# Performance work log

Measured on AMD Instinct MI355X. Metric: run time of the kernel, lower is better.

Reference implementation:

```python
import jax, jax.numpy as jnp
import numpy as np

EPS = 1e-8


def eq_linear(z, weight, bias):
    # EqualisedLinear: runtime weight scale c = 1/sqrt(in_features)
    c = 1.0 / np.sqrt(weight.shape[1]).astype(np.float32)
    return z @ (weight * c).T + bias


def mod_conv(x, w_raw, s, demodulate):
    # w_raw: [out, in, k, k], s: [b, in]
    out_c, in_c, k, _ = w_raw.shape
    c = 1.0 / np.sqrt(in_c * k * k).astype(np.float32)
    wt = w_raw * c
    # per-sample modulated weights: [b, out, in, k, k]
    ws = wt[None] * s[:, None, :, None, None]
    if demodulate:
        sigma_inv = jax.lax.rsqrt(jnp.sum(ws * ws, axis=(2, 3, 4), keepdims=True) + EPS)
        ws = ws * sigma_inv
    def conv1(xi, wi):
        return jax.lax.conv_general_dilated(
            xi[None], wi, window_strides=(1, 1), padding='SAME',
            dimension_numbers=('NCHW', 'OIHW', 'NCHW'))[0]
    return jax.vmap(conv1)(x, ws)


def lrelu(v):
    return jax.nn.leaky_relu(v, 0.2)


def style_block(x, w, noise, style_w, style_b, conv_w, noise_scale, bias):
    s = eq_linear(w, style_w, style_b)
    x = mod_conv(x, conv_w, s, demodulate=True)
    x = x + noise_scale[None, :, None, None] * noise
    return lrelu(x + bias[None, :, None, None])


def to_rgb(x, w, style_w, style_b, conv_w, bias):
    s = eq_linear(w, style_w, style_b)
    x = mod_conv(x, conv_w, s, demodulate=False)
    return lrelu(x + bias[None, :, None, None])


def setup_inputs() -> dict:
    key = jax.random.key(0)
    ks = jax.random.split(key, 16)
    B, C, H, W = 16, 512, 64, 64
    D = 512
    OUT = 3
    return {
        'x': jax.random.normal(ks[0], (B, C, H, W), jnp.float32),
        'w': jax.random.normal(ks[1], (B, D), jnp.float32),
        'noise1': jax.random.normal(ks[2], (B, 1, H, W), jnp.float32),
        'noise2': jax.random.normal(ks[3], (B, 1, H, W), jnp.float32),
        'sb1_style_w': jax.random.normal(ks[4], (C, D), jnp.float32),
        'sb1_style_b': jnp.ones((C,), jnp.float32),
        'sb1_conv_w': jax.random.normal(ks[5], (C, C, 3, 3), jnp.float32),
        'sb1_noise_scale': 0.1 * jax.random.normal(ks[6], (1,), jnp.float32),
        'sb1_bias': 0.1 * jax.random.normal(ks[7], (C,), jnp.float32),
        'sb2_style_w': jax.random.normal(ks[8], (C, D), jnp.float32),
        'sb2_style_b': jnp.ones((C,), jnp.float32),
        'sb2_conv_w': jax.random.normal(ks[9], (C, C, 3, 3), jnp.float32),
        'sb2_noise_scale': 0.1 * jax.random.normal(ks[10], (1,), jnp.float32),
        'sb2_bias': 0.1 * jax.random.normal(ks[11], (C,), jnp.float32),
        'rgb_style_w': jax.random.normal(ks[12], (C, D), jnp.float32),
        'rgb_style_b': jnp.ones((C,), jnp.float32),
        'rgb_conv_w': jax.random.normal(ks[13], (OUT, C, 1, 1), jnp.float32),
        'rgb_bias': 0.1 * jax.random.normal(ks[14], (OUT,), jnp.float32),
    }


def reference(x, w, noise1, noise2,
              sb1_style_w, sb1_style_b, sb1_conv_w, sb1_noise_scale, sb1_bias,
              sb2_style_w, sb2_style_b, sb2_conv_w, sb2_noise_scale, sb2_bias,
              rgb_style_w, rgb_style_b, rgb_conv_w, rgb_bias):
    x = style_block(x, w, noise1, sb1_style_w, sb1_style_b, sb1_conv_w, sb1_noise_scale, sb1_bias)
    x = style_block(x, w, noise2, sb2_style_w, sb2_style_b, sb2_conv_w, sb2_noise_scale, sb2_bias)
    rgb = to_rgb(x, w, rgb_style_w, rgb_style_b, rgb_conv_w, rgb_bias)
    return (x, rgb)
```

## Files before the change

kernel.cpp:

```cpp
#include <hip/hip_runtime.h>
#include <hip/hip_bf16.h>

typedef float f32x4 __attribute__((ext_vector_type(4)));
typedef short short8 __attribute__((ext_vector_type(8)));

#define CC   512
#define PIX  4096
#define XHROWBYTES 4224
#define XHBYTES    16896

__device__ __forceinline__ unsigned short f2bf(float f){
    __hip_bfloat16 h = __float2bfloat16(f);
    return __builtin_bit_cast(unsigned short, h);
}
__device__ __forceinline__ unsigned pk2(float a, float b){
    return (unsigned)f2bf(a) | ((unsigned)f2bf(b) << 16);
}
__device__ __forceinline__ void mfma_bf16(f32x4& c, short8 a, short8 b){
    asm("v_mfma_f32_16x16x32_bf16 %0, %1, %2, %0" : "+v"(c) : "v"(a), "v"(b));
}

__global__ void k_style3(const float* __restrict__ w,
                         const float* __restrict__ sw0, const float* __restrict__ sb0, float* __restrict__ o0,
                         const float* __restrict__ sw1, const float* __restrict__ sb1, float* __restrict__ o1,
                         const float* __restrict__ sw2, const float* __restrict__ sb2, float* __restrict__ o2){
    __shared__ float wl[512];
    const int b = blockIdx.x, l = blockIdx.y, tid = threadIdx.x;
    const float* sw = (l==0) ? sw0 : (l==1 ? sw1 : sw2);
    const float* sb = (l==0) ? sb0 : (l==1 ? sb1 : sb2);
    float* so       = (l==0) ? o0  : (l==1 ? o1  : o2);
    wl[tid]       = w[b*512 + tid];
    wl[tid + 256] = w[b*512 + 256 + tid];
    __syncthreads();
    const float c = 0.044194173824159216f;
    for (int cc = tid; cc < 512; cc += 256){
        const float4* row = (const float4*)(sw + cc*512);
        float acc = 0.f;
        #pragma unroll 4
        for (int dd = 0; dd < 128; ++dd){
            float4 v = row[dd];
            float4 wv = ((const float4*)wl)[dd];
            acc += v.x*wv.x + v.y*wv.y + v.z*wv.z + v.w*wv.w;
        }
        so[b*512 + cc] = acc * c + sb[cc];
    }
}

__global__ void k_w2(const float* __restrict__ cw1, const float* __restrict__ cw2,
                     float* __restrict__ w2_1, float* __restrict__ w2_2){
    int gid = blockIdx.x*256 + threadIdx.x;
    int layer = gid >> 18; int r = gid & 262143;
    const float* cw = layer ? cw2 : cw1;
    float* w2 = layer ? w2_2 : w2_1;
    const float c2 = 1.0f/4608.0f;
    const float* p = cw + r*9;
    float sum = 0.f;
    #pragma unroll
    for (int t=0;t<9;++t){ float v = p[t]; sum += v*v; }
    w2[r] = sum * c2;
}

__global__ void k_demod2(const float* __restrict__ w21, const float* __restrict__ w22,
                         const float* __restrict__ s1,  const float* __restrict__ s2,
                         float* __restrict__ d1, float* __restrict__ d2){
    __shared__ float s2l[512];
    const int b = blockIdx.x, l = blockIdx.y, o = threadIdx.x;
    const float* w2 = l ? w22 : w21;
    const float* s  = l ? s2  : s1;
    float* d        = l ? d2  : d1;
    float sv = s[b*512 + o]; s2l[o] = sv*sv;
    __syncthreads();
    const float4* row = (const float4*)(w2 + o*512);
    const float4* sq  = (const float4*)s2l;
    float acc = 0.f;
    #pragma unroll 4
    for (int i=0;i<128;++i){
        float4 a = row[i], bq = sq[i];
        acc += a.x*bq.x + a.y*bq.y + a.z*bq.z + a.w*bq.w;
    }
    d[b*512 + o] = rsqrtf(acc + 1e-8f);
}

__global__ void k_pack(const float* __restrict__ cw1, const float* __restrict__ cw2,
                       uint4* __restrict__ wpk1, uint4* __restrict__ wpk2){
    int gid = blockIdx.x*256 + threadIdx.x;
    int layer = (gid >= 294912);
    int r = layer ? gid - 294912 : gid;
    const float* cw = layer ? cw2 : cw1;
    uint4* dst = layer ? wpk2 : wpk1;
    int lane = r & 63;
    int ofr  = (r>>6) & 31;
    int cb   = (r>>11) & 15;
    int t    = r>>15;
    int o  = ofr*16 + (lane&15);
    int i0 = cb*32 + (lane>>4)*8;
    const float c = 0.014731391274719738f;
    const float* src = cw + (o*512 + i0)*9 + t;
    float f[8];
    #pragma unroll
    for (int j=0;j<8;++j) f[j] = src[j*9]*c;
    uint4 wv;
    wv.x = pk2(f[0],f[1]); wv.y = pk2(f[2],f[3]);
    wv.z = pk2(f[4],f[5]); wv.w = pk2(f[6],f[7]);
    dst[r] = wv;
}

__global__ __launch_bounds__(256, 2)
void k_conv(const float* __restrict__ x, float* __restrict__ y,
            const unsigned short* __restrict__ wpk, const float* __restrict__ s,
            const float* __restrict__ dmod, const float* __restrict__ noise,
            const float* __restrict__ nsp, const float* __restrict__ bias){
    __shared__ __align__(16) char smem[35840];
    char* xh0 = smem;
    char* xh1 = smem + XHBYTES;
    float* s_lds = (float*)(smem + 2*XHBYTES);

    const int tid  = threadIdx.x;
    const int obp  = blockIdx.x;
    const int rb   = blockIdx.y;
    const int b    = blockIdx.z;
    const int r0   = rb*2;
    const int lane = tid & 63;
    const int wv   = tid >> 6;
    const int ln15 = lane & 15;
    const int hi   = lane >> 4;

    const float* xb = x + (size_t)b * (512*PIX);

    s_lds[tid]       = s[b*512 + tid];
    s_lds[tid + 256] = s[b*512 + 256 + tid];
    __syncthreads();

    f32x4 acc[4][8];
    #pragma unroll
    for (int mi=0;mi<4;++mi)
        #pragma unroll
        for (int ni=0;ni<8;++ni) acc[mi][ni] = (f32x4)(0.f);

    unsigned bcol[3][4];
    #pragma unroll
    for (int dxi=0; dxi<3; ++dxi)
        #pragma unroll
        for (int ni=0; ni<4; ++ni){
            int xcol = ni*16 + ln15 + dxi;
            unsigned a = (unsigned)(xcol*64 + hi*16);
            a ^= (unsigned)(((xcol>>1)&3)<<4);
            bcol[dxi][ni] = a;
        }

    const int scol   = tid & 63;
    const int schunk = (tid>>6) & 3;
    unsigned wcol = (unsigned)((scol+1)*64 + schunk*16);
    wcol ^= (unsigned)((((scol+1)>>1)&3)<<4);

    auto stage = [&](int cb, char* dst){
        float sv[8];
        #pragma unroll
        for (int j=0;j<8;++j) sv[j] = s_lds[cb*32 + schunk*8 + j];
        const float* srcbase = xb + (size_t)(cb*32 + schunk*8)*PIX + scol;
        #pragma unroll
        for (int row=0; row<4; ++row){
            int gr = r0 - 1 + row;
            uint4 wq = make_uint4(0u,0u,0u,0u);
            if (0 <= gr && gr < 64){
                const float* sp = srcbase + gr*64;
                float f0 = sp[0*PIX]*sv[0], f1 = sp[1*PIX]*sv[1];
                float f2 = sp[2*PIX]*sv[2], f3 = sp[3*PIX]*sv[3];
                float f4 = sp[4*PIX]*sv[4], f5 = sp[5*PIX]*sv[5];
                float f6 = sp[6*PIX]*sv[6], f7 = sp[7*PIX]*sv[7];
                wq.x = pk2(f0,f1); wq.y = pk2(f2,f3);
                wq.z = pk2(f4,f5); wq.w = pk2(f6,f7);
            }
            *(uint4*)(dst + row*XHROWBYTES + wcol) = wq;
        }
        if (tid < 32){
            int row = tid>>3; int hc = (tid&4) ? 65 : 0; int ck = tid&3;
            unsigned a = (unsigned)((row*66 + hc)*64 + ck*16);
            a ^= (unsigned)(((hc>>1)&3)<<4);
            *(uint4*)(dst + a) = make_uint4(0u,0u,0u,0u);
        }
    };

    stage(0, xh0);

    const short8* wpf = (const short8*)wpk + (size_t)(obp*16 + wv*4)*64 + lane;

    #pragma unroll 2
    for (int cb=0; cb<16; ++cb){
        __syncthreads();
        if (cb+1 < 16) stage(cb+1, (cb&1) ? xh0 : xh1);
        const char* cur = (cb&1) ? xh1 : xh0;
        const short8* wp = wpf + (size_t)cb*(32*64);
        #pragma unroll
        for (int t=0; t<9; ++t){
            const int dxi = t%3;
            short8 Af[4];
            #pragma unroll
            for (int mi=0;mi<4;++mi) Af[mi] = wp[(size_t)t*(16*32*64) + mi*64];
            const char* rbase0 = cur + (t/3)*XHROWBYTES;
            const char* rbase1 = rbase0 + XHROWBYTES;
            short8 Bf[8];
            #pragma unroll
            for (int ni=0;ni<4;++ni) Bf[ni]   = *(const short8*)(rbase0 + bcol[dxi][ni]);
            #pragma unroll
            for (int ni=0;ni<4;++ni) Bf[4+ni] = *(const short8*)(rbase1 + bcol[dxi][ni]);
            #pragma unroll
            for (int ni=0;ni<8;++ni)
                #pragma unroll
                for (int mi=0;mi<4;++mi)
                    mfma_bf16(acc[mi][ni], Af[mi], Bf[ni]);
        }
    }

    const int obase = obp*256 + wv*64;
    const float nsv = nsp[0];
    const float* dgl = dmod + b*512 + obase;
    const float* bgl = bias + obase;
    float nz[8];
    #pragma unroll
    for (int ni=0;ni<8;++ni){
        int row = r0 + (ni>>2);
        nz[ni] = nsv * noise[b*PIX + row*64 + (ni&3)*16 + ln15];
    }
    float* yb = y + ((size_t)(b*512 + obase))*PIX;
    #pragma unroll
    for (int mi=0;mi<4;++mi){
        float dv[4], bv[4];
        #pragma unroll
        for (int r=0;r<4;++r){
            int ol = mi*16 + hi*4 + r;
            dv[r] = dgl[ol]; bv[r] = bgl[ol];
        }
        #pragma unroll
        for (int ni=0;ni<8;++ni){
            int row = r0 + (ni>>2);
            int col = (ni&3)*16 + ln15;
            #pragma unroll
            for (int r=0;r<4;++r){
                float v = acc[mi][ni][r]*dv[r] + nz[ni] + bv[r];
                v = fmaxf(v, 0.2f*v);
                yb[(size_t)(mi*16 + hi*4 + r)*PIX + row*64 + col] = v;
            }
        }
    }
}

__global__ void k_rgb(const float* __restrict__ x2, const float* __restrict__ srgb,
                      const float* __restrict__ cw, const float* __restrict__ bias,
                      float* __restrict__ out){
    __shared__ float4 wr[512];
    const int b = blockIdx.x, tid = threadIdx.x;
    const float c = 0.044194173824159216f;
    for (int cc = tid; cc < 512; cc += 256){
        float sc = srgb[b*512 + cc]*c;
        wr[cc] = make_float4(cw[cc]*sc, cw[512+cc]*sc, cw[1024+cc]*sc, 0.f);
    }
    __syncthreads();
    int px = blockIdx.y*256 + tid;
    const float* xp = x2 + (size_t)b*(512*PIX) + px;
    float a0=0.f, a1=0.f, a2=0.f;
    #pragma unroll 4
    for (int i=0;i<512;++i){
        float xv = xp[(size_t)i*PIX];
        float4 wv = wr[i];
        a0 += wv.x*xv; a1 += wv.y*xv; a2 += wv.z*xv;
    }
    a0 += bias[0]; a1 += bias[1]; a2 += bias[2];
    out[(size_t)(b*3+0)*PIX + px] = fmaxf(a0, 0.2f*a0);
    out[(size_t)(b*3+1)*PIX + px] = fmaxf(a1, 0.2f*a1);
    out[(size_t)(b*3+2)*PIX + px] = fmaxf(a2, 0.2f*a2);
}

extern "C" void kernel_launch(void* const* d_in, const int* in_sizes, int n_in,
                              void* d_out, int out_size, void* d_ws, size_t ws_size,
                              hipStream_t stream) {
    const float* x    = (const float*)d_in[0];
    const float* w    = (const float*)d_in[1];
    const float* n1   = (const float*)d_in[2];
    const float* n2   = (const float*)d_in[3];
    const float* s1w  = (const float*)d_in[4];
    const float* s1b  = (const float*)d_in[5];
    const float* c1w  = (const float*)d_in[6];
    const float* ns1  = (const float*)d_in[7];
    const float* b1   = (const float*)d_in[8];
    const float* s2w  = (const float*)d_in[9];
    const float* s2b  = (const float*)d_in[10];
    const float* c2w  = (const float*)d_in[11];
    const float* ns2  = (const float*)d_in[12];
    const float* b2   = (const float*)d_in[13];
    const float* rw   = (const float*)d_in[14];
    const float* rbv  = (const float*)d_in[15];
    const float* rcw  = (const float*)d_in[16];
    const float* rbias= (const float*)d_in[17];

    float* out_x   = (float*)d_out;
    float* out_rgb = out_x + (size_t)16*512*PIX;

    char* ws = (char*)d_ws;
    float* s1   = (float*)(ws + 0);
    float* s2   = (float*)(ws + 32768);
    float* srgb = (float*)(ws + 65536);
    float* d1   = (float*)(ws + 98304);
    float* d2   = (float*)(ws + 131072);
    float* w21  = (float*)(ws + 163840);
    float* w22  = (float*)(ws + 163840 + 1048576);
    unsigned short* wp1 = (unsigned short*)(ws + 2260992);
    unsigned short* wp2 = wp1 + 2359296;
    float* x1   = (float*)(ws + 11698176);

    k_style3<<<dim3(16,3), 256, 0, stream>>>(w, s1w, s1b, s1, s2w, s2b, s2, rw, rbv, srgb);
    k_w2<<<2048, 256, 0, stream>>>(c1w, c2w, w21, w22);
    k_pack<<<2304, 256, 0, stream>>>(c1w, c2w, (uint4*)wp1, (uint4*)wp2);
    k_demod2<<<dim3(16,2), 512, 0, stream>>>(w21, w22, s1, s2, d1, d2);

    dim3 cg(2, 32, 16);
    k_conv<<<cg, 256, 0, stream>>>(x,  x1,    wp1, s1, d1, n1, ns1, b1);
    k_conv<<<cg, 256, 0, stream>>>(x1, out_x, wp2, s2, d2, n2, ns2, b2);
    k_rgb<<<dim3(16,16), 256, 0, stream>>>(out_x, srgb, rcw, rbias, out_rgb);
}
```

Measured before the change: 797.0 us.

## Pre-stage modulated bf16 halo tiles globally and DMA them into LDS

Adds a separate k_stage_g pass that applies the style scale, converts x to bf16 and writes swizzled, padded 6-row halo tiles to workspace. k_conv then copies its 4-row window into LDS with global_load_lds direct transfers rather than doing per-thread fp32 loads, scaling and packing. This is meant to remove the staging ALU work and the redundant fp32 reads from the conv's main loop. The cost is an extra kernel launch and global write/read traffic for the packed tiles. It also hoists the first tap's weight loads ahead of the staging call, and the layer-1 output now goes to out_x instead of a separate buffer.

Result: slower. 839.5 us (+5.3%).

```diff
diff --git a/kernel.cpp b/kernel.cpp
--- a/kernel.cpp
+++ b/kernel.cpp
@@ -4,10 +4,11 @@
 typedef float f32x4 __attribute__((ext_vector_type(4)));
 typedef short short8 __attribute__((ext_vector_type(8)));
 
-#define CC   512
-#define PIX  4096
-#define XHROWBYTES 4224
-#define XHBYTES    16896
+#define CC    512
+#define PIX   4096
+#define ROWB  4224
+#define TILE6 25344
+#define TILE4 16896
 
 __device__ __forceinline__ unsigned short f2bf(float f){
     __hip_bfloat16 h = __float2bfloat16(f);
@@ -18,6 +19,11 @@
 }
 __device__ __forceinline__ void mfma_bf16(f32x4& c, short8 a, short8 b){
     asm("v_mfma_f32_16x16x32_bf16 %0, %1, %2, %0" : "+v"(c) : "v"(a), "v"(b));
+}
+__device__ __forceinline__ void gl_lds16(const void* g, void* l){
+    __builtin_amdgcn_global_load_lds(
+        (const __attribute__((address_space(1))) unsigned int*)g,
+        (__attribute__((address_space(3))) unsigned int*)l, 16, 0, 0);
 }
 
 __global__ void k_style3(const float* __restrict__ w,
@@ -105,61 +111,28 @@
     dst[r] = wv;
 }
 
-__global__ __launch_bounds__(256, 2)
-void k_conv(const float* __restrict__ x, float* __restrict__ y,
-            const unsigned short* __restrict__ wpk, const float* __restrict__ s,
-            const float* __restrict__ dmod, const float* __restrict__ noise,
-            const float* __restrict__ nsp, const float* __restrict__ bias){
-    __shared__ __align__(16) char smem[35840];
-    char* xh0 = smem;
-    char* xh1 = smem + XHBYTES;
-    float* s_lds = (float*)(smem + 2*XHBYTES);
-
-    const int tid  = threadIdx.x;
-    const int obp  = blockIdx.x;
-    const int rb   = blockIdx.y;
-    const int b    = blockIdx.z;
-    const int r0   = rb*2;
-    const int lane = tid & 63;
-    const int wv   = tid >> 6;
-    const int ln15 = lane & 15;
-    const int hi   = lane >> 4;
-
-    const float* xb = x + (size_t)b * (512*PIX);
-
+__global__ void k_stage_g(const float* __restrict__ x, const float* __restrict__ s,
+                          char* __restrict__ xpg){
+    __shared__ float s_lds[512];
+    const int tid = threadIdx.x;
+    const int rb = blockIdx.x, b = blockIdx.y;
+    const int r0 = rb*4;
     s_lds[tid]       = s[b*512 + tid];
     s_lds[tid + 256] = s[b*512 + 256 + tid];
     __syncthreads();
-
-    f32x4 acc[4][8];
-    #pragma unroll
-    for (int mi=0;mi<4;++mi)
-        #pragma unroll
-        for (int ni=0;ni<8;++ni) acc[mi][ni] = (f32x4)(0.f);
-
-    unsigned bcol[3][4];
-    #pragma unroll
-    for (int dxi=0; dxi<3; ++dxi)
-        #pragma unroll
-        for (int ni=0; ni<4; ++ni){
-            int xcol = ni*16 + ln15 + dxi;
-            unsigned a = (unsigned)(xcol*64 + hi*16);
-            a ^= (unsigned)(((xcol>>1)&3)<<4);
-            bcol[dxi][ni] = a;
-        }
-
     const int scol   = tid & 63;
     const int schunk = (tid>>6) & 3;
     unsigned wcol = (unsigned)((scol+1)*64 + schunk*16);
     wcol ^= (unsigned)((((scol+1)>>1)&3)<<4);
-
-    auto stage = [&](int cb, char* dst){
+    const float* xb = x + (size_t)b * (512*PIX);
+    for (int cb=0; cb<16; ++cb){
+        char* dst = xpg + ((size_t)((b*16 + rb)*16 + cb))*TILE6;
         float sv[8];
         #pragma unroll
         for (int j=0;j<8;++j) sv[j] = s_lds[cb*32 + schunk*8 + j];
         const float* srcbase = xb + (size_t)(cb*32 + schunk*8)*PIX + scol;
         #pragma unroll
-        for (int row=0; row<4; ++row){
+        for (int row=0; row<6; ++row){
             int gr = r0 - 1 + row;
             uint4 wq = make_uint4(0u,0u,0u,0u);
             if (0 <= gr && gr < 64){
@@ -171,14 +144,62 @@
                 wq.x = pk2(f0,f1); wq.y = pk2(f2,f3);
                 wq.z = pk2(f4,f5); wq.w = pk2(f6,f7);
             }
-            *(uint4*)(dst + row*XHROWBYTES + wcol) = wq;
-        }
-        if (tid < 32){
+            *(uint4*)(dst + row*ROWB + wcol) = wq;
+        }
+        if (tid < 48){
             int row = tid>>3; int hc = (tid&4) ? 65 : 0; int ck = tid&3;
             unsigned a = (unsigned)((row*66 + hc)*64 + ck*16);
             a ^= (unsigned)(((hc>>1)&3)<<4);
             *(uint4*)(dst + a) = make_uint4(0u,0u,0u,0u);
         }
+    }
+}
+
+__global__ __launch_bounds__(256, 2)
+void k_conv(const char* __restrict__ xpg, float* __restrict__ y,
+            const unsigned short* __restrict__ wpk,
+            const float* __restrict__ dmod, const float* __restrict__ noise,
+            const float* __restrict__ nsp, const float* __restrict__ bias){
+    __shared__ __align__(16) char smem[2*TILE4];
+    char* xh0 = smem;
+    char* xh1 = smem + TILE4;
+
+    const int tid  = threadIdx.x;
+    const int obp  = blockIdx.x;
+    const int rb   = blockIdx.y;
+    const int b    = blockIdx.z;
+    const int r0   = rb*2;
+    const int lane = tid & 63;
+    const int wv   = tid >> 6;
+    const int ln15 = lane & 15;
+    const int hi   = lane >> 4;
+
+    f32x4 acc[4][8];
+    #pragma unroll
+    for (int mi=0;mi<4;++mi)
+        #pragma unroll
+        for (int ni=0;ni<8;++ni) acc[mi][ni] = (f32x4)(0.f);
+
+    unsigned bcol[3][4];
+    #pragma unroll
+    for (int dxi=0; dxi<3; ++dxi)
+        #pragma unroll
+        for (int ni=0; ni<4; ++ni){
+            int xcol = ni*16 + ln15 + dxi;
+            unsigned a = (unsigned)(xcol*64 + hi*16);
+            a ^= (unsigned)(((xcol>>1)&3)<<4);
+            bcol[dxi][ni] = a;
+        }
+
+    const char* tbase = xpg + ((size_t)((b*16 + (rb>>1))*16))*TILE6
+                            + (size_t)(rb&1)*2*ROWB;
+    auto stage = [&](int cb2, char* dstb){
+        const char* src = tbase + (size_t)cb2*TILE6;
+        #pragma unroll
+        for (int k=0;k<4;++k)
+            gl_lds16(src + (size_t)(tid + k*256)*16, dstb + (tid + k*256)*16);
+        if (tid < 32)
+            gl_lds16(src + (size_t)(1024 + tid)*16, dstb + (1024 + tid)*16);
     };
 
     stage(0, xh0);
@@ -188,17 +209,21 @@
     #pragma unroll 2
     for (int cb=0; cb<16; ++cb){
         __syncthreads();
+        const short8* wp = wpf + (size_t)cb*(32*64);
+        short8 Af[4];
+        #pragma unroll
+        for (int mi=0;mi<4;++mi) Af[mi] = wp[mi*64];
         if (cb+1 < 16) stage(cb+1, (cb&1) ? xh0 : xh1);
         const char* cur = (cb&1) ? xh1 : xh0;
-        const short8* wp = wpf + (size_t)cb*(32*64);
         #pragma unroll
         for (int t=0; t<9; ++t){
             const int dxi = t%3;
-            short8 Af[4];
-            #pragma unroll
-            for (int mi=0;mi<4;++mi) Af[mi] = wp[(size_t)t*(16*32*64) + mi*64];
-            const char* rbase0 = cur + (t/3)*XHROWBYTES;
-            const char* rbase1 = rbase0 + XHROWBYTES;
+            if (t > 0){
+                #pragma unroll
+                for (int mi=0;mi<4;++mi) Af[mi] = wp[(size_t)t*(16*32*64) + mi*64];
+            }
+            const char* rbase0 = cur + (t/3)*ROWB;
+            const char* rbase1 = rbase0 + ROWB;
             short8 Bf[8];
             #pragma unroll
             for (int ni=0;ni<4;++ni) Bf[ni]   = *(const short8*)(rbase0 + bcol[dxi][ni]);
@@ -306,7 +331,8 @@
     float* w22  = (float*)(ws + 163840 + 1048576);
     unsigned short* wp1 = (unsigned short*)(ws + 2260992);
     unsigned short* wp2 = wp1 + 2359296;
-    float* x1   = (float*)(ws + 11698176);
+    char* xpg   = ws + 11698176;
+    float* x1   = out_x;
 
     k_style3<<<dim3(16,3), 256, 0, stream>>>(w, s1w, s1b, s1, s2w, s2b, s2, rw, rbv, srgb);
     k_w2<<<2048, 256, 0, stream>>>(c1w, c2w, w21, w22);
@@ -314,7 +340,9 @@
     k_demod2<<<dim3(16,2), 512, 0, stream>>>(w21, w22, s1, s2, d1, d2);
 
     dim3 cg(2, 32, 16);
-    k_conv<<<cg, 256, 0, stream>>>(x,  x1,    wp1, s1, d1, n1, ns1, b1);
-    k_conv<<<cg, 256, 0, stream>>>(x1, out_x, wp2, s2, d2, n2, ns2, b2);
+    k_stage_g<<<dim3(16,16), 256, 0, stream>>>(x, s1, xpg);
+    k_conv<<<cg, 256, 0, stream>>>(xpg, x1, wp1, d1, n1, ns1, b1);
+    k_stage_g<<<dim3(16,16), 256, 0, stream>>>(x1, s2, xpg);
+    k_conv<<<cg, 256, 0, stream>>>(xpg, out_x, wp2, d2, n2, ns2, b2);
     k_rgb<<<dim3(16,16), 256, 0, stream>>>(out_x, srgb, rcw, rbias, out_rgb);
 }
```
